# Kernel tuning notes

Hardware: AMD Instinct MI355X
Metric: run time of the kernel (lower is better)

Reference implementation:

```python
import jax, jax.numpy as jnp
import numpy as np

B, S, D = 4, 2048, 1024

def setup_inputs() -> dict:
    key = jax.random.key(0)
    k1, k2, k3, k4 = jax.random.split(key, 4)
    x = jax.random.normal(k1, (B, S, D), dtype=jnp.float32)
    # module init: jr.normal(key, (dim, dim)) / 40
    Qw = jax.random.normal(k2, (D, D), dtype=jnp.float32) / 40
    Kw = jax.random.normal(k3, (D, D), dtype=jnp.float32) / 40
    Vw = jax.random.normal(k4, (D, D), dtype=jnp.float32) / 40
    return {"x": x, "Qw": Qw, "Kw": Kw, "Vw": Vw}

def reference(x, Qw, Kw, Vw):
    # Q/K/V projections: [B,S,D] @ [D,D] -> [B,S,D]
    Q = x @ Qw
    K = x @ Kw
    V = x @ Vw
    d = x.shape[-1]
    S_len = x.shape[-2]
    # causal additive mask: 0 on/below diagonal, -inf above
    mask = jnp.where(jnp.tril(jnp.ones((S_len, S_len), dtype=x.dtype)) == 0,
                     -jnp.inf, 0.0).astype(x.dtype)
    # scores: [B,S,S]
    scores = jnp.einsum('bqd,bkd->bqk', Q, K) / jnp.sqrt(jnp.asarray(d, x.dtype))
    scores = scores + mask
    attn = jax.nn.softmax(scores, axis=-1)
    return jnp.einsum('bqk,bkd->bqd', attn, V)
```

## Files before the change

### kernel.cpp

```cpp
#include <hip/hip_runtime.h>
#include <hip/hip_bf16.h>

typedef __attribute__((ext_vector_type(8))) __bf16 bf16x8;
typedef __attribute__((ext_vector_type(8))) short short8;
typedef __attribute__((ext_vector_type(4))) float f32x4;

#define BK 64

__device__ inline unsigned short f2bf(float f) {
    union { float f; unsigned u; } v; v.f = f;
    unsigned r = (v.u + 0x7FFFu + ((v.u >> 16) & 1u)) >> 16;
    return (unsigned short)r;
}

__device__ __forceinline__ void gld16(const void* g, void* l) {
    __builtin_amdgcn_global_load_lds(
        (const __attribute__((address_space(1))) unsigned int*)g,
        (__attribute__((address_space(3))) unsigned int*)l, 16, 0, 0);
}

__device__ inline int detect_dt(const unsigned short* x, int tid, int* red)
{
    int cnt = 0;
    for (int i = tid; i < 1024; i += 256) {
        unsigned e = (x[2 * i] >> 7) & 0xFFu;
        cnt += (e >= 0x60u && e <= 0x88u) ? 1 : 0;
    }
    #pragma unroll
    for (int o = 32; o >= 1; o >>= 1) cnt += __shfl_xor(cnt, o, 64);
    if ((tid & 63) == 0) red[tid >> 6] = cnt;
    __syncthreads();
    return (red[0] + red[1] + red[2] + red[3] >= 512) ? 0 : 1;
}

__global__ void detect_dtype(const unsigned short* __restrict__ x, int* __restrict__ flag)
{
    __shared__ int red[4];
    const int dt = detect_dt(x, threadIdx.x, red);
    if (threadIdx.x == 0) *flag = dt;
}

__global__ __launch_bounds__(256)
void prep(const void* __restrict__ x, const void* __restrict__ Qw,
          const void* __restrict__ Kw, const void* __restrict__ Vw,
          unsigned short* __restrict__ Xb, unsigned short* __restrict__ QwB,
          unsigned short* __restrict__ KwB, unsigned short* __restrict__ VwT,
          long nX, long nW, int Dd, int* __restrict__ dtf)
{
    const int bid = blockIdx.x;
    const int tid = threadIdx.x;
    __shared__ int red[4];
    const int dt = detect_dt((const unsigned short*)x, tid, red);
    if (bid == 0 && tid == 0) *dtf = dt;

    const int nbX = (int)(nX >> 11);
    const int nbW = (int)(nW >> 11);
    __shared__ unsigned short tbuf[64][65];

    if (bid < nbX + 2 * nbW) {
        const void* s; unsigned short* d; long i;
        if (bid < nbX)            { s = x;  d = Xb;  i = ((long)bid << 11) + tid * 8; }
        else if (bid < nbX + nbW) { s = Qw; d = QwB; i = ((long)(bid - nbX) << 11) + tid * 8; }
        else                      { s = Kw; d = KwB; i = ((long)(bid - nbX - nbW) << 11) + tid * 8; }
        union { short8 v; unsigned short u[8]; } o;
        if (dt) {
            f32x4 a = *(const f32x4*)((const float*)s + i);
            f32x4 b = *(const f32x4*)((const float*)s + i + 4);
            #pragma unroll
            for (int j = 0; j < 4; j++) { o.u[j] = f2bf(a[j]); o.u[4 + j] = f2bf(b[j]); }
        } else {
            o.v = *(const short8*)((const short*)s + i);
        }
        *(short8*)(d + i) = o.v;
        return;
    }
    const int t64 = bid - (nbX + 2 * nbW);
    const int c0 = (t64 & 15) * 64, r0 = (t64 >> 4) * 64;
    #pragma unroll
    for (int it = 0; it < 16; it++) {
        int idx = it * 256 + tid;
        int r = idx >> 6, c = idx & 63;
        long e = (long)(r0 + r) * Dd + (c0 + c);
        tbuf[r][c] = dt ? f2bf(((const float*)Vw)[e]) : ((const unsigned short*)Vw)[e];
    }
    __syncthreads();
    #pragma unroll
    for (int it = 0; it < 16; it++) {
        int idx = it * 256 + tid;
        int r = idx >> 6, c = idx & 63;
        VwT[(long)(c0 + r) * Dd + (r0 + c)] = tbuf[c][r];
    }
}

template <int TM>
__global__ __launch_bounds__(256, 2)
void gemm_bt(const unsigned short* __restrict__ A, const unsigned short* __restrict__ Bt,
             void* __restrict__ Call, int K, int lda, int ldb, int ldc,
             long oA, long oB, long oC, long sA, long sB, long sC,
             float scale, int mode, int q0,
             const int* __restrict__ dtf, int outKind,
             const unsigned short* __restrict__ Bt2, void* __restrict__ C2)
{
    constexpr int NI = TM / 32;
    const int dt = *dtf;
    int zSel = blockIdx.z;
    if (mode != 3 && Bt2 && zSel) { Bt = Bt2; Call = C2; }

    int mt, nt;
    if (mode == 3) {
        const int lin = blockIdx.x;
        const int j = (lin < 256) ? lin : 767 - lin;
        mt = 15 - (j >> 5);
        zSel = (j >> 3) & 3;
        nt = j & 7;
    } else if (mode == 2) {
        const int nwg2 = gridDim.x * gridDim.y;
        const int h = blockIdx.y * gridDim.x + blockIdx.x;
        const int u = h >> 1;
        const int rank = (h & 1) ? (nwg2 - 1 - u) : u;
        mt = (gridDim.y - 1) - (rank / (int)gridDim.x);
        nt = rank % (int)gridDim.x;
    } else {
        const int nwg = gridDim.x * gridDim.y;
        int lin = blockIdx.y * gridDim.x + blockIdx.x;
        const int q = nwg >> 3, r = nwg & 7;
        const int xcd = lin & 7, idx = lin >> 3;
        lin = (xcd < r ? xcd * (q + 1) : r * (q + 1) + (xcd - r) * q) + idx;
        if (mode == 1) {
            int rem = lin, rr = 0, w = q0 / TM + 1;
            while (rem >= w) { rem -= w; rr++; w++; }
            mt = rr; nt = rem;
        } else { mt = lin / gridDim.x; nt = lin % gridDim.x; }
    }
    const long aBase = oA + (long)zSel * sA;
    const long bBase = oB + (long)zSel * sB;
    const long cBase = oC + (long)zSel * sC;
    const int m0 = mt * TM;
    const int n0 = nt * TM;
    int kmax = K;
    if (mode >= 2) kmax = min(K, q0 + m0 + TM);

    __shared__ __align__(16) short As[2][TM * BK];
    __shared__ __align__(16) short Bs[2][TM * BK];

    const int tid  = threadIdx.x;
    const int wave = tid >> 6;
    const int lane = tid & 63;
    const int wm = (wave >> 1) * (TM / 2);
    const int wn = (wave & 1) * (TM / 2);
    const int lrow = lane & 15;
    const int quad = lane >> 4;

    const int sRow = lane >> 3;
    const int sCol = ((lane & 7) ^ sRow) * 8;
    const long gA = aBase + (long)(m0 + wave * (TM / 4) + sRow) * lda + sCol;
    const long gB = bBase + (long)(n0 + wave * (TM / 4) + sRow) * ldb + sCol;

    auto stage = [&](int buf, int k0) {
        short* dA = &As[buf][wave * (TM / 4) * BK];
        short* dB = &Bs[buf][wave * (TM / 4) * BK];
        const unsigned short* pA = A + gA + k0;
        const unsigned short* pB = Bt + gB + k0;
        #pragma unroll
        for (int c = 0; c < TM / 32; c++) {
            gld16(pA + (long)(c * 8) * lda, dA + c * 8 * BK);
            gld16(pB + (long)(c * 8) * ldb, dB + c * 8 * BK);
        }
    };

    f32x4 acc[NI][NI];
    #pragma unroll
    for (int i = 0; i < NI; i++)
        #pragma unroll
        for (int j = 0; j < NI; j++) {
            f32x4 zero = {0.f, 0.f, 0.f, 0.f};
            acc[i][j] = zero;
        }

    const int rq  = lrow & 7;
    const int pc0 = (quad ^ rq) * 8;
    const int pc1 = ((quad + 4) ^ rq) * 8;

    stage(0, 0);
    __syncthreads();
    int cur = 0;

    for (int k0 = 0; k0 < kmax; k0 += BK) {
        const int kn = k0 + BK;
        if (kn < kmax) stage(cur ^ 1, kn);

        const short* rA = &As[cur][0];
        const short* rB = &Bs[cur][0];
        bf16x8 af[NI], bfr[NI];
        #pragma unroll
        for (int i = 0; i < NI; i++) {
            af[i]  = *(const bf16x8*)&rA[(wm + i * 16 + lrow) * BK + pc0];
            bfr[i] = *(const bf16x8*)&rB[(wn + i * 16 + lrow) * BK + pc0];
        }
        #pragma unroll
        for (int i = 0; i < NI; i++)
            #pragma unroll
            for (int j = 0; j < NI; j++)
                acc[i][j] = __builtin_amdgcn_mfma_f32_16x16x32_bf16(af[i], bfr[j], acc[i][j], 0, 0, 0);
        #pragma unroll
        for (int i = 0; i < NI; i++) {
            af[i]  = *(const bf16x8*)&rA[(wm + i * 16 + lrow) * BK + pc1];
            bfr[i] = *(const bf16x8*)&rB[(wn + i * 16 + lrow) * BK + pc1];
        }
        #pragma unroll
        for (int i = 0; i < NI; i++)
            #pragma unroll
            for (int j = 0; j < NI; j++)
                acc[i][j] = __builtin_amdgcn_mfma_f32_16x16x32_bf16(af[i], bfr[j], acc[i][j], 0, 0, 0);

        __syncthreads();
        cur ^= 1;
    }

    const int oF32 = (outKind == 1) | ((outKind == 2) & dt);
    #pragma unroll
    for (int i = 0; i < NI; i++) {
        const int mr = m0 + wm + i * 16 + quad * 4;
        #pragma unroll
        for (int j = 0; j < NI; j++) {
            const int nc = n0 + wn + j * 16 + lrow;
            #pragma unroll
            for (int r = 0; r < 4; r++) {
                const long ofs = cBase + (long)(mr + r) * ldc + nc;
                const float v = acc[i][j][r] * scale;
                if (oF32) ((float*)Call)[ofs] = v;
                else      ((unsigned short*)Call)[ofs] = f2bf(v);
            }
        }
    }
}

__global__ __launch_bounds__(256)
void xpose_cast(const void* __restrict__ src, unsigned short* __restrict__ dT,
                unsigned short* __restrict__ dC, int R, int C,
                long oS, long sS, long sDT, long sDC,
                const int* __restrict__ dtf, int srcExt)
{
    const int dt = srcExt ? *dtf : 0;
    const int b = blockIdx.z;
    const long sb = oS + (long)b * sS;
    __shared__ unsigned short t[64][65];
    const int c0 = blockIdx.x * 64, r0 = blockIdx.y * 64;
    const int tid = threadIdx.x;
    #pragma unroll
    for (int it = 0; it < 16; it++) {
        int idx = it * 256 + tid;
        int r = idx >> 6, c = idx & 63;
        long e = sb + (long)(r0 + r) * C + (c0 + c);
        unsigned short v = dt ? f2bf(((const float*)src)[e]) : ((const unsigned short*)src)[e];
        t[r][c] = v;
        if (dC) dC[(long)b * sDC + (long)(r0 + r) * C + (c0 + c)] = v;
    }
    if (!dT) return;
    __syncthreads();
    #pragma unroll
    for (int it = 0; it < 16; it++) {
        int idx = it * 256 + tid;
        int r = idx >> 6, c = idx & 63;
        dT[(long)b * sDT + (long)(c0 + r) * R + (r0 + c)] = t[c][r];
    }
}

__global__ __launch_bounds__(256)
void softmax_causal(float* __restrict__ Sc, int S, int CH, int q0)
{
    const int r = blockIdx.x, z = blockIdx.y;
    float* srow = Sc + ((long)z * CH + r) * S;
    unsigned short* prow = (unsigned short*)srow;
    const int n = q0 + r + 1;
    const int limit = q0 + (r & ~127) + 128;
    const int tid = threadIdx.x;
    const int lane = tid & 63, wave = tid >> 6;
    const int j0 = tid * 8;
    __shared__ float red[4];

    float v[8];
    {
        f32x4 a = *(const f32x4*)(srow + j0);
        f32x4 b = *(const f32x4*)(srow + j0 + 4);
        #pragma unroll
        for (int c = 0; c < 4; c++) { v[c] = a[c]; v[4 + c] = b[c]; }
    }
    float lm = -1e30f;
    #pragma unroll
    for (int c = 0; c < 8; c++) {
        v[c] = (j0 + c < n) ? v[c] : -1e30f;
        lm = fmaxf(lm, v[c]);
    }
    #pragma unroll
    for (int o = 32; o >= 1; o >>= 1) lm = fmaxf(lm, __shfl_xor(lm, o, 64));
    if (lane == 0) red[wave] = lm;
    __syncthreads();
    const float m = fmaxf(fmaxf(red[0], red[1]), fmaxf(red[2], red[3]));
    __syncthreads();

    float ev[8];
    float ls = 0.f;
    #pragma unroll
    for (int c = 0; c < 8; c++) {
        float e = (j0 + c < n) ? __expf(v[c] - m) : 0.f;
        ev[c] = e;
        ls += e;
    }
    #pragma unroll
    for (int o = 32; o >= 1; o >>= 1) ls += __shfl_xor(ls, o, 64);
    if (lane == 0) red[wave] = ls;
    __syncthreads();
    const float inv = 1.0f / (red[0] + red[1] + red[2] + red[3]);

    if (j0 < limit) {
        union { short8 s; unsigned short u[8]; } o;
        #pragma unroll
        for (int c = 0; c < 8; c++) o.u[c] = f2bf(ev[c] * inv);
        *(short8*)(prow + j0) = o.s;
    }
}

__global__ __launch_bounds__(256)
void fill_zero(void* o, long n, const int* dtf)
{
    long i = (long)blockIdx.x * 256 + threadIdx.x;
    if (i < n) {
        if (*dtf) ((float*)o)[i] = 0.f;
        else ((unsigned short*)o)[i] = 0;
    }
}

extern "C" void kernel_launch(void* const* d_in, const int* in_sizes, int n_in,
                              void* d_out, int out_size, void* d_ws, size_t ws_size,
                              hipStream_t stream)
{
    const int B = 4, S = 2048, D = 1024;
    const void* x  = d_in[0];
    const void* Qw = d_in[1];
    const void* Kw = d_in[2];
    const void* Vw = d_in[3];
    (void)in_sizes; (void)n_in; (void)out_size;

    int* dtf = (int*)d_ws;
    char* p = (char*)d_ws + 4096;
    const size_t MB = (size_t)1 << 20;
    const unsigned short* nullB = nullptr;

    const long nOut = (long)B * S * D;
    const long nX = (long)B * S * D;
    const long nW = (long)D * D;
    const int prepBlocks = (int)(nX >> 11) + 2 * (int)(nW >> 11) + (D / 64) * (D / 64);

    const size_t needAp = 4096 + 52 * MB + (size_t)B * S * S * 4;
    if (ws_size >= needAp) {
        unsigned short* QwB = (unsigned short*)p;
        unsigned short* KwB = (unsigned short*)(p + 2 * MB);
        unsigned short* Xb  = (unsigned short*)(p + 4 * MB);
        unsigned short* Buf = (unsigned short*)(p + 20 * MB);
        unsigned short* VbT = (unsigned short*)(p + 36 * MB);
        float* Sc = (float*)(p + 52 * MB);
        unsigned short* WT  = (unsigned short*)Sc;
        unsigned short* VwT = (unsigned short*)((char*)Sc + 2 * MB);

        prep<<<dim3(prepBlocks), 256, 0, stream>>>(
            x, Qw, Kw, Vw, Xb, QwB, KwB, VwT, nX, nW, D, dtf);
        gemm_bt<64><<<dim3(16, 16, 1), 256, 0, stream>>>(
            KwB, QwB, WT, D, D, D, D, 0L, 0L, 0L, 0L, 0L, 0L,
            0.03125f, 0, 0, dtf, 0, nullB, nullptr);
        gemm_bt<128><<<dim3(16, 8, 4), 256, 0, stream>>>(
            VwT, Xb, VbT, D, D, D, S,
            0L, 0L, 0L, 0L, (long)S * D, (long)D * S,
            1.0f, 0, 0, dtf, 0, nullB, nullptr);
        gemm_bt<128><<<dim3(8, 64, 1), 256, 0, stream>>>(
            Xb, WT, Buf, D, D, D, D, 0L, 0L, 0L, 0L, 0L, 0L,
            1.0f, 0, 0, dtf, 0, nullB, nullptr);
        gemm_bt<128><<<dim3(136, 1, 4), 256, 0, stream>>>(
            Buf, Xb, (void*)Sc, D, D, D, S,
            0L, 0L, 0L, (long)S * D, (long)S * D, (long)S * S,
            1.0f, 1, 0, dtf, 1, nullB, nullptr);
        softmax_causal<<<dim3(S, 4), 256, 0, stream>>>(Sc, S, S, 0);
        gemm_bt<128><<<dim3(512, 1, 1), 256, 0, stream>>>(
            (const unsigned short*)Sc, VbT, d_out, S, 2 * S, S, D,
            0L, 0L, 0L, (long)2 * S * S, (long)D * S, (long)S * D,
            1.0f, 3, 0, dtf, 2, nullB, nullptr);
        return;
    }

    const size_t needA = 4096 + 36 * MB + (size_t)B * S * S * 4;
    if (ws_size >= needA) {
        unsigned short* QwB = (unsigned short*)p;
        unsigned short* KwB = (unsigned short*)(p + 2 * MB);
        unsigned short* Xb  = (unsigned short*)(p + 4 * MB);
        unsigned short* Buf = (unsigned short*)(p + 20 * MB);
        float* Sc = (float*)(p + 36 * MB);
        unsigned short* WT  = (unsigned short*)Sc;
        unsigned short* VwT = (unsigned short*)((char*)Sc + 2 * MB);
        unsigned short* VbT = Xb;
        unsigned short* VbS = (unsigned short*)d_out;

        prep<<<dim3(prepBlocks), 256, 0, stream>>>(
            x, Qw, Kw, Vw, Xb, QwB, KwB, VwT, nX, nW, D, dtf);
        gemm_bt<64><<<dim3(16, 16, 1), 256, 0, stream>>>(
            KwB, QwB, WT, D, D, D, D, 0L, 0L, 0L, 0L, 0L, 0L,
            0.03125f, 0, 0, dtf, 0, nullB, nullptr);
        gemm_bt<128><<<dim3(8, 64, 2), 256, 0, stream>>>(
            Xb, WT, Buf, D, D, D, D, 0L, 0L, 0L, 0L, 0L, 0L,
            1.0f, 0, 0, dtf, 0, VwT, VbS);
        gemm_bt<128><<<dim3(136, 1, 4), 256, 0, stream>>>(
            Buf, Xb, (void*)Sc, D, D, D, S,
            0L, 0L, 0L, (long)S * D, (long)S * D, (long)S * S,
            1.0f, 1, 0, dtf, 1, nullB, nullptr);
        softmax_causal<<<dim3(S, 4), 256, 0, stream>>>(Sc, S, S, 0);
        xpose_cast<<<dim3(16, 32, 4), 256, 0, stream>>>(
            VbS, VbT, nullptr, S, D, 0L, (long)S * D, (long)D * S, 0L, dtf, 0);
        gemm_bt<128><<<dim3(512, 1, 1), 256, 0, stream>>>(
            (const unsigned short*)Sc, VbT, d_out, S, 2 * S, S, D,
            0L, 0L, 0L, (long)2 * S * S, (long)D * S, (long)S * D,
            1.0f, 3, 0, dtf, 2, nullB, nullptr);
        return;
    }

    const int cfgs[6][2] = {{4,1024},{2,1024},{1,1024},{1,512},{1,256},{1,128}};
    int ZB = 0, CH = 0;
    for (int i = 0; i < 6; i++) {
        size_t need = 4096 + 56 * MB + (size_t)cfgs[i][0] * cfgs[i][1] * S * 4;
        if (need <= ws_size) { ZB = cfgs[i][0]; CH = cfgs[i][1]; break; }
    }
    if (ZB == 0) {
        detect_dtype<<<1, 256, 0, stream>>>((const unsigned short*)x, dtf);
        fill_zero<<<dim3((unsigned)((nOut + 255) / 256)), 256, 0, stream>>>(d_out, nOut, dtf);
        return;
    }

    unsigned short* QwB = (unsigned short*)p;
    unsigned short* KwB = (unsigned short*)(p + 2 * MB);
    unsigned short* WT  = (unsigned short*)(p + 4 * MB);
    unsigned short* VwT = (unsigned short*)(p + 6 * MB);
    unsigned short* Xb  = (unsigned short*)(p + 8 * MB);
    unsigned short* VbT = (unsigned short*)(p + 24 * MB);
    unsigned short* Buf = (unsigned short*)(p + 40 * MB);
    float* Sc = (float*)(p + 56 * MB);
    unsigned short* VbS = (unsigned short*)d_out;

    prep<<<dim3(prepBlocks), 256, 0, stream>>>(
        x, Qw, Kw, Vw, Xb, QwB, KwB, VwT, nX, nW, D, dtf);
    gemm_bt<64><<<dim3(16, 16, 1), 256, 0, stream>>>(
        KwB, QwB, WT, D, D, D, D, 0L, 0L, 0L, 0L, 0L, 0L,
        0.03125f, 0, 0, dtf, 0, nullB, nullptr);
    gemm_bt<128><<<dim3(8, 64, 2), 256, 0, stream>>>(
        Xb, WT, Buf, D, D, D, D, 0L, 0L, 0L, 0L, 0L, 0L,
        1.0f, 0, 0, dtf, 0, VwT, VbS);
    xpose_cast<<<dim3(16, 32, 4), 256, 0, stream>>>(
        VbS, VbT, nullptr, S, D, 0L, (long)S * D, (long)D * S, 0L, dtf, 0);

    for (int b0 = 0; b0 < B; b0 += ZB) {
        for (int q0 = 0; q0 < S; q0 += CH) {
            const int base = q0 / 128, R = CH / 128;
            const int ntiles = R * (base + 1) + R * (R - 1) / 2;

            gemm_bt<128><<<dim3(ntiles, 1, ZB), 256, 0, stream>>>(
                Buf, Xb, (void*)Sc, D, D, D, S,
                (long)b0 * S * D + (long)q0 * D, (long)b0 * S * D, 0L,
                (long)S * D, (long)S * D, (long)CH * S,
                1.0f, 1, q0, dtf, 1, nullB, nullptr);

            softmax_causal<<<dim3(CH, ZB), 256, 0, stream>>>(Sc, S, CH, q0);

            gemm_bt<128><<<dim3(8, CH / 128, ZB), 256, 0, stream>>>(
                (const unsigned short*)Sc, VbT, d_out, S, 2 * S, S, D,
                0L, (long)b0 * D * S, (long)b0 * S * D + (long)q0 * D,
                (long)CH * 2 * S, (long)D * S, (long)S * D,
                1.0f, 2, q0, dtf, 2, nullB, nullptr);
        }
    }
}
```

Baseline: 252.6 us.

## Store causal scores in bf16 and merge projection GEMMs into one launch

The scores matrix is now written by the QK GEMM as bf16 instead of fp32, and a new softmax kernel normalises it in place in bf16, so the PV GEMM reads a half-size bf16 matrix with stride S. The X·WT projection and the per-batch V projection are merged into a single launch (mode 4) with an XCD-aware block remap, which removes a launch and fills the device better. This cuts memory traffic for the score write, softmax and PV read. The cost is an extra bf16 rounding of the pre-softmax scores, which may slightly reduce accuracy.

Measured after the change: 248.1 us. No clear change (-1.8%).

```diff
diff --git a/kernel.cpp b/kernel.cpp
--- a/kernel.cpp
+++ b/kernel.cpp
@@ -99,15 +99,28 @@
              long oA, long oB, long oC, long sA, long sB, long sC,
              float scale, int mode, int q0,
              const int* __restrict__ dtf, int outKind,
-             const unsigned short* __restrict__ Bt2, void* __restrict__ C2)
+             const unsigned short* __restrict__ Bt2, void* __restrict__ C2,
+             const unsigned short* __restrict__ A2, int ldc2)
 {
     constexpr int NI = TM / 32;
     const int dt = *dtf;
     int zSel = blockIdx.z;
-    if (mode != 3 && Bt2 && zSel) { Bt = Bt2; Call = C2; }
+    if (mode == 0 && Bt2 && zSel) { Bt = Bt2; Call = C2; }
 
     int mt, nt;
-    if (mode == 3) {
+    if (mode == 4) {
+        int lin = blockIdx.x;
+        const int xcd = lin & 7, idx = lin >> 3;
+        lin = xcd * 128 + idx;
+        if (lin < 512) { mt = lin >> 3; nt = lin & 7; zSel = 0; }
+        else {
+            const int j2 = lin - 512;
+            zSel = j2 >> 7;
+            const int r2 = j2 & 127;
+            mt = r2 >> 4; nt = r2 & 15;
+            A = A2; Bt = Bt2; Call = C2; ldc = ldc2;
+        }
+    } else if (mode == 3) {
         const int lin = blockIdx.x;
         const int j = (lin < 256) ? lin : 767 - lin;
         mt = 15 - (j >> 5);
@@ -138,7 +151,7 @@
     const int m0 = mt * TM;
     const int n0 = nt * TM;
     int kmax = K;
-    if (mode >= 2) kmax = min(K, q0 + m0 + TM);
+    if (mode == 2 || mode == 3) kmax = min(K, q0 + m0 + TM);
 
     __shared__ __align__(16) short As[2][TM * BK];
     __shared__ __align__(16) short Bs[2][TM * BK];
@@ -322,6 +335,63 @@
 }
 
 __global__ __launch_bounds__(256)
+void softmax_causal_b16(unsigned short* __restrict__ Sc, int S, int CH, int q0)
+{
+    const int r = blockIdx.x, z = blockIdx.y;
+    unsigned short* row = Sc + ((long)z * CH + r) * S;
+    const int n = q0 + r + 1;
+    const int limit = q0 + (r & ~127) + 128;
+    const int tid = threadIdx.x;
+    const int lane = tid & 63, wave = tid >> 6;
+    const int j0 = tid * 8;
+    __shared__ float red[4];
+
+    float v[8];
+    if (j0 < limit) {
+        union { short8 s; unsigned short u[8]; } in;
+        in.s = *(const short8*)(row + j0);
+        #pragma unroll
+        for (int c = 0; c < 8; c++) {
+            union { unsigned u; float f; } w; w.u = (unsigned)in.u[c] << 16;
+            v[c] = (j0 + c < n) ? w.f : -1e30f;
+        }
+    } else {
+        #pragma unroll
+        for (int c = 0; c < 8; c++) v[c] = -1e30f;
+    }
+    float lm = -1e30f;
+    #pragma unroll
+    for (int c = 0; c < 8; c++) lm = fmaxf(lm, v[c]);
+    #pragma unroll
+    for (int o = 32; o >= 1; o >>= 1) lm = fmaxf(lm, __shfl_xor(lm, o, 64));
+    if (lane == 0) red[wave] = lm;
+    __syncthreads();
+    const float m = fmaxf(fmaxf(red[0], red[1]), fmaxf(red[2], red[3]));
+    __syncthreads();
+
+    float ev[8];
+    float ls = 0.f;
+    #pragma unroll
+    for (int c = 0; c < 8; c++) {
+        float e = (j0 + c < n) ? __expf(v[c] - m) : 0.f;
+        ev[c] = e;
+        ls += e;
+    }
+    #pragma unroll
+    for (int o = 32; o >= 1; o >>= 1) ls += __shfl_xor(ls, o, 64);
+    if (lane == 0) red[wave] = ls;
+    __syncthreads();
+    const float inv = 1.0f / (red[0] + red[1] + red[2] + red[3]);
+
+    if (j0 < limit) {
+        union { short8 s; unsigned short u[8]; } o;
+        #pragma unroll
+        for (int c = 0; c < 8; c++) o.u[c] = f2bf(ev[c] * inv);
+        *(short8*)(row + j0) = o.s;
+    }
+}
+
+__global__ __launch_bounds__(256)
 void fill_zero(void* o, long n, const int* dtf)
 {
     long i = (long)blockIdx.x * 256 + threadIdx.x;
@@ -352,38 +422,35 @@
     const long nW = (long)D * D;
     const int prepBlocks = (int)(nX >> 11) + 2 * (int)(nW >> 11) + (D / 64) * (D / 64);
 
-    const size_t needAp = 4096 + 52 * MB + (size_t)B * S * S * 4;
+    const size_t needAp = 4096 + 52 * MB + (size_t)B * S * S * 2;
     if (ws_size >= needAp) {
         unsigned short* QwB = (unsigned short*)p;
         unsigned short* KwB = (unsigned short*)(p + 2 * MB);
         unsigned short* Xb  = (unsigned short*)(p + 4 * MB);
         unsigned short* Buf = (unsigned short*)(p + 20 * MB);
         unsigned short* VbT = (unsigned short*)(p + 36 * MB);
-        float* Sc = (float*)(p + 52 * MB);
-        unsigned short* WT  = (unsigned short*)Sc;
+        unsigned short* Sc  = (unsigned short*)(p + 52 * MB);
+        unsigned short* WT  = Sc;
         unsigned short* VwT = (unsigned short*)((char*)Sc + 2 * MB);
 
         prep<<<dim3(prepBlocks), 256, 0, stream>>>(
             x, Qw, Kw, Vw, Xb, QwB, KwB, VwT, nX, nW, D, dtf);
         gemm_bt<64><<<dim3(16, 16, 1), 256, 0, stream>>>(
             KwB, QwB, WT, D, D, D, D, 0L, 0L, 0L, 0L, 0L, 0L,
-            0.03125f, 0, 0, dtf, 0, nullB, nullptr);
-        gemm_bt<128><<<dim3(16, 8, 4), 256, 0, stream>>>(
-            VwT, Xb, VbT, D, D, D, S,
+            0.03125f, 0, 0, dtf, 0, nullB, nullptr, nullB, 0);
+        gemm_bt<128><<<dim3(1024, 1, 1), 256, 0, stream>>>(
+            Xb, WT, Buf, D, D, D, D,
             0L, 0L, 0L, 0L, (long)S * D, (long)D * S,
-            1.0f, 0, 0, dtf, 0, nullB, nullptr);
-        gemm_bt<128><<<dim3(8, 64, 1), 256, 0, stream>>>(
-            Xb, WT, Buf, D, D, D, D, 0L, 0L, 0L, 0L, 0L, 0L,
-            1.0f, 0, 0, dtf, 0, nullB, nullptr);
+            1.0f, 4, 0, dtf, 0, Xb, VbT, VwT, S);
         gemm_bt<128><<<dim3(136, 1, 4), 256, 0, stream>>>(
-            Buf, Xb, (void*)Sc, D, D, D, S,
+            Buf, Xb, Sc, D, D, D, S,
             0L, 0L, 0L, (long)S * D, (long)S * D, (long)S * S,
-            1.0f, 1, 0, dtf, 1, nullB, nullptr);
-        softmax_causal<<<dim3(S, 4), 256, 0, stream>>>(Sc, S, S, 0);
+            1.0f, 1, 0, dtf, 0, nullB, nullptr, nullB, 0);
+        softmax_causal_b16<<<dim3(S, 4), 256, 0, stream>>>(Sc, S, S, 0);
         gemm_bt<128><<<dim3(512, 1, 1), 256, 0, stream>>>(
-            (const unsigned short*)Sc, VbT, d_out, S, 2 * S, S, D,
-            0L, 0L, 0L, (long)2 * S * S, (long)D * S, (long)S * D,
-            1.0f, 3, 0, dtf, 2, nullB, nullptr);
+            Sc, VbT, d_out, S, S, S, D,
+            0L, 0L, 0L, (long)S * S, (long)D * S, (long)S * D,
+            1.0f, 3, 0, dtf, 2, nullB, nullptr, nullB, 0);
         return;
     }
 
@@ -403,21 +470,21 @@
             x, Qw, Kw, Vw, Xb, QwB, KwB, VwT, nX, nW, D, dtf);
         gemm_bt<64><<<dim3(16, 16, 1), 256, 0, stream>>>(
             KwB, QwB, WT, D, D, D, D, 0L, 0L, 0L, 0L, 0L, 0L,
-            0.03125f, 0, 0, dtf, 0, nullB, nullptr);
+            0.03125f, 0, 0, dtf, 0, nullB, nullptr, nullB, 0);
         gemm_bt<128><<<dim3(8, 64, 2), 256, 0, stream>>>(
             Xb, WT, Buf, D, D, D, D, 0L, 0L, 0L, 0L, 0L, 0L,
-            1.0f, 0, 0, dtf, 0, VwT, VbS);
+            1.0f, 0, 0, dtf, 0, VwT, VbS, nullB, 0);
         gemm_bt<128><<<dim3(136, 1, 4), 256, 0, stream>>>(
             Buf, Xb, (void*)Sc, D, D, D, S,
             0L, 0L, 0L, (long)S * D, (long)S * D, (long)S * S,
-            1.0f, 1, 0, dtf, 1, nullB, nullptr);
+            1.0f, 1, 0, dtf, 1, nullB, nullptr, nullB, 0);
         softmax_causal<<<dim3(S, 4), 256, 0, stream>>>(Sc, S, S, 0);
         xpose_cast<<<dim3(16, 32, 4), 256, 0, stream>>>(
             VbS, VbT, nullptr, S, D, 0L, (long)S * D, (long)D * S, 0L, dtf, 0);
         gemm_bt<128><<<dim3(512, 1, 1), 256, 0, stream>>>(
             (const unsigned short*)Sc, VbT, d_out, S, 2 * S, S, D,
             0L, 0L, 0L, (long)2 * S * S, (long)D * S, (long)S * D,
-            1.0f, 3, 0, dtf, 2, nullB, nullptr);
+            1.0f, 3, 0, dtf, 2, nullB, nullptr, nullB, 0);
         return;
     }
 
@@ -447,10 +514,10 @@
         x, Qw, Kw, Vw, Xb, QwB, KwB, VwT, nX, nW, D, dtf);
     gemm_bt<64><<<dim3(16, 16, 1), 256, 0, stream>>>(
         KwB, QwB, WT, D, D, D, D, 0L, 0L, 0L, 0L, 0L, 0L,
-        0.03125f, 0, 0, dtf, 0, nullB, nullptr);
+        0.03125f, 0, 0, dtf, 0, nullB, nullptr, nullB, 0);
     gemm_bt<128><<<dim3(8, 64, 2), 256, 0, stream>>>(
         Xb, WT, Buf, D, D, D, D, 0L, 0L, 0L, 0L, 0L, 0L,
-        1.0f, 0, 0, dtf, 0, VwT, VbS);
+        1.0f, 0, 0, dtf, 0, VwT, VbS, nullB, 0);
     xpose_cast<<<dim3(16, 32, 4), 256, 0, stream>>>(
         VbS, VbT, nullptr, S, D, 0L, (long)S * D, (long)D * S, 0L, dtf, 0);
 
@@ -463,7 +530,7 @@
                 Buf, Xb, (void*)Sc, D, D, D, S,
                 (long)b0 * S * D + (long)q0 * D, (long)b0 * S * D, 0L,
                 (long)S * D, (long)S * D, (long)CH * S,
-                1.0f, 1, q0, dtf, 1, nullB, nullptr);
+                1.0f, 1, q0, dtf, 1, nullB, nullptr, nullB, 0);
 
             softmax_causal<<<dim3(CH, ZB), 256, 0, stream>>>(Sc, S, CH, q0);
 
@@ -471,7 +538,7 @@
                 (const unsigned short*)Sc, VbT, d_out, S, 2 * S, S, D,
                 0L, (long)b0 * D * S, (long)b0 * S * D + (long)q0 * D,
                 (long)CH * 2 * S, (long)D * S, (long)S * D,
-                1.0f, 2, q0, dtf, 2, nullB, nullptr);
-        }
-    }
-}
+                1.0f, 2, q0, dtf, 2, nullB, nullptr, nullB, 0);
+        }
+    }
+}
```
